# Optimization experiments

Hardware: AMD Instinct MI355X
Metric: run time of the kernel (lower is better)

## Reference

```python
import jax, jax.numpy as jnp
import numpy as np

TAU = 1.0
SCALE = 0.5
LN_EPS = 1e-5
NORM_EPS = 1e-12


def setup_inputs() -> dict:
    key = jax.random.key(0)
    k1, = jax.random.split(key, 1)
    N, D = 16384, 128
    x = jax.random.normal(k1, (N, D), dtype=jnp.float32)
    gamma = jnp.ones((D,), dtype=jnp.float32)
    beta = jnp.zeros((D,), dtype=jnp.float32)
    return {"x": x, "gamma": gamma, "beta": beta}


def reference(x, gamma, beta):
    # 'cn' branch: row-normalize, full pairwise cosine sim, row softmax, aggregate
    norm = jnp.sqrt(jnp.sum(x * x, axis=1, keepdims=True))
    norm_x = x / jnp.maximum(norm, NORM_EPS)          # [N, D]
    sim = jax.nn.softmax(norm_x @ norm_x.T / TAU, axis=1)  # [N, N]
    x_neg = sim @ x                                    # [N, D]
    y = (1.0 + SCALE) * x - SCALE * x_neg
    # LayerNorm over the hidden dim
    mu = jnp.mean(y, axis=-1, keepdims=True)
    var = jnp.mean((y - mu) ** 2, axis=-1, keepdims=True)
    return (y - mu) * jax.lax.rsqrt(var + LN_EPS) * gamma + beta
```

## Files before the change

### kernel.cpp

```cpp
#include <hip/hip_runtime.h>
#include <stdint.h>

#define NN 16384
#define DD 128
#define KT 64
#define QB 128
#define VSTR 72
#define VBYTES 9216

typedef float f32x16 __attribute__((ext_vector_type(16)));
typedef int i32x8 __attribute__((ext_vector_type(8)));

using gv = __attribute__((address_space(1))) const void;
using lv = __attribute__((address_space(3))) void;

__device__ __forceinline__ i32x8 mk8(uint4 a, uint4 b) {
  i32x8 r;
  r[0] = a.x; r[1] = a.y; r[2] = a.z; r[3] = a.w;
  r[4] = b.x; r[5] = b.y; r[6] = b.z; r[7] = b.w;
  return r;
}

#define MFMA64(A, B, C) \
  __builtin_amdgcn_mfma_scale_f32_32x32x64_f8f6f4((A), (B), (C), 0, 0, 0, 0x7F7F7F7F, 0, 0x7F7F7F7F)

__global__ void k_norm(const float* __restrict__ x, uint8_t* __restrict__ nx) {
  const int wave = threadIdx.x >> 6, lane = threadIdx.x & 63;
  const int row = blockIdx.x * 4 + wave;
  const float2 v = *reinterpret_cast<const float2*>(x + (size_t)row * DD + 2 * lane);
  float ss = v.x * v.x + v.y * v.y;
#pragma unroll
  for (int m = 1; m < 64; m <<= 1) ss += __shfl_xor(ss, m);
  const float rn = 1.2011224087f / fmaxf(sqrtf(ss), 1e-12f);
  const int w = __builtin_amdgcn_cvt_pk_fp8_f32(v.x * rn, v.y * rn, 0, false);
  *reinterpret_cast<uint16_t*>(nx + (size_t)row * DD + 2 * lane) = (uint16_t)w;
}

__global__ void k_transpose(const float* __restrict__ x, uint8_t* __restrict__ xT) {
  __shared__ uint16_t tile[64 * 66];
  const int n0 = blockIdx.x * 64;
  const int t = threadIdx.x;
#pragma unroll
  for (int e = 0; e < 16; ++e) {
    const int idx = e * 256 + t;
    const int r = idx >> 6, c2 = idx & 63;
    const float2 v = *reinterpret_cast<const float2*>(x + (size_t)(n0 + r) * DD + 2 * c2);
    const int w = __builtin_amdgcn_cvt_pk_fp8_f32(v.x, v.y, 0, false);
    tile[r * 66 + c2] = (uint16_t)w;
  }
  __syncthreads();
  const uint8_t* t8 = reinterpret_cast<const uint8_t*>(tile);
#pragma unroll
  for (int e = 0; e < 8; ++e) {
    const int idx = e * 256 + t;
    const int d = idx >> 4, n4 = (idx & 15) << 2;
    uint32_t w = (uint32_t)t8[(n4 + 0) * 132 + d];
    w |= (uint32_t)t8[(n4 + 1) * 132 + d] << 8;
    w |= (uint32_t)t8[(n4 + 2) * 132 + d] << 16;
    w |= (uint32_t)t8[(n4 + 3) * 132 + d] << 24;
    *reinterpret_cast<uint32_t*>(xT + (size_t)d * NN + n0 + n4) = w;
  }
}

template <int NSPLIT>
__global__ __launch_bounds__(256, 3) void k_attn(
    const uint8_t* __restrict__ nx, const uint8_t* __restrict__ xT,
    float* __restrict__ Op, float* __restrict__ Lp) {
  __shared__ alignas(16) uint8_t Vb[2][VBYTES];

  const int tid = threadIdx.x;
  const int wave = tid >> 6;
  const int lane = tid & 63;
  const int rl = lane & 31;
  const int hi = lane >> 5;

  const int id = blockIdx.x;
  const int split = id >> 7;
  const int qblock = id & 127;

  constexpr int qtn = 256 / NSPLIT;
  constexpr int rem = 256 % NSPLIT;
  const int nt = qtn + (split < rem ? 1 : 0);
  const int t0s = split * qtn + (split < rem ? split : rem);

  const int qw = qblock * QB + wave * 32;

  const int j0 = 2 * wave;
  const int cnt = (wave == 3) ? 3 : 2;
  uint32_t soff[3];
#pragma unroll
  for (int i = 0; i < 3; ++i) {
    const int j = j0 + i;
    const int t16 = j * 64 + lane;
    const int d = (2 * t16) / 9;
    const int c0 = t16 * 16 - d * VSTR;
    soff[i] = (uint32_t)(d * NN + c0 + (c0 >= 64 ? (NN - VSTR) : 0));
  }

  auto stage = [&](int tt, int buf) {
    const uint8_t* basep = xT + tt * KT;
#pragma unroll
    for (int i = 0; i < 3; ++i)
      if (i < cnt)
        __builtin_amdgcn_global_load_lds((gv*)(basep + soff[i]),
            (lv*)(&Vb[buf][0] + (j0 + i) * 1024), 16, 0, 0);
  };

  const uint8_t* qrow = nx + (size_t)(qw + rl) * DD + 32 * hi;
  i32x8 q8[2];
#pragma unroll
  for (int c = 0; c < 2; ++c)
    q8[c] = mk8(*reinterpret_cast<const uint4*>(qrow + c * 64),
                *reinterpret_cast<const uint4*>(qrow + c * 64 + 16));

  f32x16 o[4];
#pragma unroll
  for (int dt = 0; dt < 4; ++dt)
#pragma unroll
    for (int r = 0; r < 16; ++r) o[dt][r] = 0.f;
  float lsum = 0.f;

  stage(t0s, 0);

  for (int t = 0; t < nt; ++t) {
    const int buf = t & 1;
    __builtin_amdgcn_sched_barrier(0);
    asm volatile("s_waitcnt vmcnt(0)" ::: "memory");
    __builtin_amdgcn_sched_barrier(0);
    __builtin_amdgcn_s_barrier();
    __builtin_amdgcn_sched_barrier(0);
    if (t + 1 < nt) stage(t0s + t + 1, buf ^ 1);

    const int k0 = (t0s + t) * KT;
    const uint8_t* vb = &Vb[buf][0];
    const uint8_t* kgp = nx + (size_t)k0 * DD + (size_t)rl * DD + 32 * hi;

    uint32_t W0[4], W1[4];
#pragma unroll
    for (int kt = 0; kt < 2; ++kt) {
      const uint8_t* kp = kgp + kt * 32 * DD;
      const i32x8 ka0 = mk8(*reinterpret_cast<const uint4*>(kp),
                            *reinterpret_cast<const uint4*>(kp + 16));
      const i32x8 ka1 = mk8(*reinterpret_cast<const uint4*>(kp + 64),
                            *reinterpret_cast<const uint4*>(kp + 80));
      f32x16 s = {};
      __builtin_amdgcn_s_setprio(1);
      s = MFMA64(ka0, q8[0], s);
      s = MFMA64(ka1, q8[1], s);
      __builtin_amdgcn_s_setprio(0);
      float e[16];
#pragma unroll
      for (int r = 0; r < 16; ++r) {
        float p;
        asm("v_exp_f32 %0, %1" : "=v"(p) : "v"(s[r]));
        e[r] = p;
        lsum += p;
      }
      uint32_t* W = kt ? W1 : W0;
#pragma unroll
      for (int g = 0; g < 4; ++g) {
        uint32_t w = (uint32_t)__builtin_amdgcn_cvt_pk_fp8_f32(e[4 * g + 0], e[4 * g + 1], 0, false);
        w = (uint32_t)__builtin_amdgcn_cvt_pk_fp8_f32(e[4 * g + 2], e[4 * g + 3], (int)w, true);
        W[g] = w;
      }
    }
#pragma unroll
    for (int g = 0; g < 4; ++g)
      asm("v_permlane32_swap_b32 %0, %1" : "+v"(W0[g]), "+v"(W1[g]));
    i32x8 pa;
    pa[0] = (int)W0[0]; pa[1] = (int)W1[0]; pa[2] = (int)W0[1]; pa[3] = (int)W1[1];
    pa[4] = (int)W0[2]; pa[5] = (int)W1[2]; pa[6] = (int)W0[3]; pa[7] = (int)W1[3];

    __builtin_amdgcn_s_setprio(1);
#pragma unroll
    for (int dt = 0; dt < 4; ++dt) {
      const uint8_t* vp = vb + (dt * 32 + rl) * VSTR + 32 * hi;
      const i32x8 vf = mk8(*reinterpret_cast<const uint4*>(vp),
                           *reinterpret_cast<const uint4*>(vp + 16));
      o[dt] = MFMA64(pa, vf, o[dt]);
    }
    __builtin_amdgcn_s_setprio(0);
  }

  const float lt = lsum + __shfl_xor(lsum, 32);
  if (hi == 0) Lp[(size_t)split * NN + qw + rl] = lt;

  float* Ob = Op + (size_t)split * NN * DD;
#pragma unroll
  for (int dt = 0; dt < 4; ++dt)
#pragma unroll
    for (int r = 0; r < 16; ++r) {
      const int q = (r & 3) + 8 * (r >> 2) + 4 * hi;
      Ob[(size_t)(qw + q) * DD + dt * 32 + rl] = o[dt][r];
    }
}

__global__ void k_final(const float* __restrict__ x, const float* __restrict__ gamma,
                        const float* __restrict__ beta, const float* __restrict__ Op,
                        const float* __restrict__ Lp, float* __restrict__ out, int nsplit) {
  const int wave = threadIdx.x >> 6, lane = threadIdx.x & 63;
  const int row = blockIdx.x * 4 + wave;
  float o0 = 0.f, o1 = 0.f, lt = 0.f;
  for (int s = 0; s < nsplit; ++s) {
    const float2 v = *reinterpret_cast<const float2*>(
        Op + (size_t)s * NN * DD + (size_t)row * DD + 2 * lane);
    o0 += v.x;
    o1 += v.y;
    lt += Lp[(size_t)s * NN + row];
  }
  const float inv = 1.0f / lt;
  const float2 xv = *reinterpret_cast<const float2*>(x + (size_t)row * DD + 2 * lane);
  float y0 = 1.5f * xv.x - 0.5f * o0 * inv;
  float y1 = 1.5f * xv.y - 0.5f * o1 * inv;
  float sum = y0 + y1;
#pragma unroll
  for (int m = 1; m < 64; m <<= 1) sum += __shfl_xor(sum, m);
  const float mu = sum * (1.0f / 128.0f);
  const float d0 = y0 - mu, d1 = y1 - mu;
  float vs = d0 * d0 + d1 * d1;
#pragma unroll
  for (int m = 1; m < 64; m <<= 1) vs += __shfl_xor(vs, m);
  const float rs = rsqrtf(vs * (1.0f / 128.0f) + 1e-5f);
  const float2 g = *reinterpret_cast<const float2*>(gamma + 2 * lane);
  const float2 b = *reinterpret_cast<const float2*>(beta + 2 * lane);
  float2 ov;
  ov.x = d0 * rs * g.x + b.x;
  ov.y = d1 * rs * g.y + b.y;
  *reinterpret_cast<float2*>(out + (size_t)row * DD + 2 * lane) = ov;
}

extern "C" void kernel_launch(void* const* d_in, const int* in_sizes, int n_in,
                              void* d_out, int out_size, void* d_ws, size_t ws_size,
                              hipStream_t stream) {
  const float* x = (const float*)d_in[0];
  const float* gamma = (const float*)d_in[1];
  const float* beta = (const float*)d_in[2];
  float* out = (float*)d_out;
  char* ws = (char*)d_ws;

  uint8_t* nx = (uint8_t*)ws;
  uint8_t* xT = (uint8_t*)(ws + (size_t)NN * DD);
  const size_t base = (size_t)2 * NN * DD;
  const size_t per = (size_t)NN * DD * 4 + (size_t)NN * 4;

  int nsplit = 2;
  if (ws_size >= base + 6 * per) nsplit = 6;
  else if (ws_size >= base + 4 * per) nsplit = 4;

  float* Op = (float*)(ws + base);
  float* Lp = (float*)(ws + base + (size_t)nsplit * NN * DD * 4);

  k_norm<<<NN / 4, 256, 0, stream>>>(x, nx);
  k_transpose<<<NN / 64, 256, 0, stream>>>(x, xT);
  if (nsplit == 6)
    k_attn<6><<<dim3(128 * 6), 256, 0, stream>>>(nx, xT, Op, Lp);
  else if (nsplit == 4)
    k_attn<4><<<dim3(128 * 4), 256, 0, stream>>>(nx, xT, Op, Lp);
  else
    k_attn<2><<<dim3(128 * 2), 256, 0, stream>>>(nx, xT, Op, Lp);
  k_final<<<NN / 4, 256, 0, stream>>>(x, gamma, beta, Op, Lp, out, nsplit);
}
```

Measured before the change: 163.0 us.

## Stage K tiles through LDS, raise occupancy, use 8 splits with grouped block mapping

Each K tile is now brought into a double-buffered LDS buffer with global_load_lds alongside the V tile. Two waves stage K while the other two stage V, so the per-wave global fragment loads in the inner loop go away. Occupancy in launch bounds goes from 3 to 4, the split-K count goes from 6 to 8 with a block index mapping that groups splits of the same query block together, and the setprio hints are removed. This doubles LDS use per block and could hurt if the extra LDS traffic or the larger partial-output reduction outweighs the gain in reuse.

New measurement: 165.6 us. Within noise of the previous version (+1.6%).

```diff
diff --git a/kernel.cpp b/kernel.cpp
--- a/kernel.cpp
+++ b/kernel.cpp
@@ -5,7 +5,9 @@
 #define DD 128
 #define KT 64
 #define QB 128
+#define KSTR 144
 #define VSTR 72
+#define KBYTES 9216
 #define VBYTES 9216
 
 typedef float f32x16 __attribute__((ext_vector_type(16)));
@@ -63,9 +65,10 @@
 }
 
 template <int NSPLIT>
-__global__ __launch_bounds__(256, 3) void k_attn(
+__global__ __launch_bounds__(256, 4) void k_attn(
     const uint8_t* __restrict__ nx, const uint8_t* __restrict__ xT,
     float* __restrict__ Op, float* __restrict__ Lp) {
+  __shared__ alignas(16) uint8_t Kb[2][KBYTES];
   __shared__ alignas(16) uint8_t Vb[2][VBYTES];
 
   const int tid = threadIdx.x;
@@ -75,35 +78,40 @@
   const int hi = lane >> 5;
 
   const int id = blockIdx.x;
-  const int split = id >> 7;
-  const int qblock = id & 127;
-
-  constexpr int qtn = 256 / NSPLIT;
-  constexpr int rem = 256 % NSPLIT;
-  const int nt = qtn + (split < rem ? 1 : 0);
-  const int t0s = split * qtn + (split < rem ? split : rem);
-
+  constexpr int gs = 8 / NSPLIT;
+  const int split = (id & 7) / gs;
+  const int qblock = (id >> 3) * gs + (id & (gs - 1));
+
+  constexpr int nt = 256 / NSPLIT;
+  const int t0s = split * nt;
   const int qw = qblock * QB + wave * 32;
 
-  const int j0 = 2 * wave;
-  const int cnt = (wave == 3) ? 3 : 2;
-  uint32_t soff[3];
-#pragma unroll
-  for (int i = 0; i < 3; ++i) {
+  const int sw = wave >> 1;
+  const int j0 = (wave & 1) * 5;
+  const int cnt = (wave & 1) ? 4 : 5;
+  uint32_t soff[5];
+#pragma unroll
+  for (int i = 0; i < 5; ++i) {
     const int j = j0 + i;
     const int t16 = j * 64 + lane;
-    const int d = (2 * t16) / 9;
-    const int c0 = t16 * 16 - d * VSTR;
-    soff[i] = (uint32_t)(d * NN + c0 + (c0 >= 64 ? (NN - VSTR) : 0));
+    if (sw == 0) {
+      soff[i] = (uint32_t)((t16 / 9) * DD + (t16 % 9) * 16);
+    } else {
+      const int d = (2 * t16) / 9;
+      const int c0 = t16 * 16 - d * VSTR;
+      soff[i] = (uint32_t)(d * NN + c0 + (c0 >= 64 ? (NN - VSTR) : 0));
+    }
   }
 
   auto stage = [&](int tt, int buf) {
-    const uint8_t* basep = xT + tt * KT;
-#pragma unroll
-    for (int i = 0; i < 3; ++i)
+    const int k0 = tt * KT;
+    const uint8_t* basep = (sw == 0) ? (nx + (size_t)k0 * DD) : (xT + k0);
+    uint8_t* ldsb = (sw == 0) ? &Kb[buf][0] : &Vb[buf][0];
+#pragma unroll
+    for (int i = 0; i < 5; ++i)
       if (i < cnt)
         __builtin_amdgcn_global_load_lds((gv*)(basep + soff[i]),
-            (lv*)(&Vb[buf][0] + (j0 + i) * 1024), 16, 0, 0);
+            (lv*)(ldsb + (j0 + i) * 1024), 16, 0, 0);
   };
 
   const uint8_t* qrow = nx + (size_t)(qw + rl) * DD + 32 * hi;
@@ -131,23 +139,20 @@
     __builtin_amdgcn_sched_barrier(0);
     if (t + 1 < nt) stage(t0s + t + 1, buf ^ 1);
 
-    const int k0 = (t0s + t) * KT;
+    const uint8_t* kb = &Kb[buf][0];
     const uint8_t* vb = &Vb[buf][0];
-    const uint8_t* kgp = nx + (size_t)k0 * DD + (size_t)rl * DD + 32 * hi;
 
     uint32_t W0[4], W1[4];
 #pragma unroll
     for (int kt = 0; kt < 2; ++kt) {
-      const uint8_t* kp = kgp + kt * 32 * DD;
-      const i32x8 ka0 = mk8(*reinterpret_cast<const uint4*>(kp),
-                            *reinterpret_cast<const uint4*>(kp + 16));
-      const i32x8 ka1 = mk8(*reinterpret_cast<const uint4*>(kp + 64),
-                            *reinterpret_cast<const uint4*>(kp + 80));
+      const uint8_t* kbb = kb + kt * 32 * KSTR + rl * KSTR + 32 * hi;
+      const i32x8 ka0 = mk8(*reinterpret_cast<const uint4*>(kbb),
+                            *reinterpret_cast<const uint4*>(kbb + 16));
+      const i32x8 ka1 = mk8(*reinterpret_cast<const uint4*>(kbb + 64),
+                            *reinterpret_cast<const uint4*>(kbb + 80));
       f32x16 s = {};
-      __builtin_amdgcn_s_setprio(1);
       s = MFMA64(ka0, q8[0], s);
       s = MFMA64(ka1, q8[1], s);
-      __builtin_amdgcn_s_setprio(0);
       float e[16];
 #pragma unroll
       for (int r = 0; r < 16; ++r) {
@@ -171,7 +176,6 @@
     pa[0] = (int)W0[0]; pa[1] = (int)W1[0]; pa[2] = (int)W0[1]; pa[3] = (int)W1[1];
     pa[4] = (int)W0[2]; pa[5] = (int)W1[2]; pa[6] = (int)W0[3]; pa[7] = (int)W1[3];
 
-    __builtin_amdgcn_s_setprio(1);
 #pragma unroll
     for (int dt = 0; dt < 4; ++dt) {
       const uint8_t* vp = vb + (dt * 32 + rl) * VSTR + 32 * hi;
@@ -179,7 +183,6 @@
                            *reinterpret_cast<const uint4*>(vp + 16));
       o[dt] = MFMA64(pa, vf, o[dt]);
     }
-    __builtin_amdgcn_s_setprio(0);
   }
 
   const float lt = lsum + __shfl_xor(lsum, 32);
@@ -244,7 +247,7 @@
   const size_t per = (size_t)NN * DD * 4 + (size_t)NN * 4;
 
   int nsplit = 2;
-  if (ws_size >= base + 6 * per) nsplit = 6;
+  if (ws_size >= base + 8 * per) nsplit = 8;
   else if (ws_size >= base + 4 * per) nsplit = 4;
 
   float* Op = (float*)(ws + base);
@@ -252,8 +255,8 @@
 
   k_norm<<<NN / 4, 256, 0, stream>>>(x, nx);
   k_transpose<<<NN / 64, 256, 0, stream>>>(x, xT);
-  if (nsplit == 6)
-    k_attn<6><<<dim3(128 * 6), 256, 0, stream>>>(nx, xT, Op, Lp);
+  if (nsplit == 8)
+    k_attn<8><<<dim3(128 * 8), 256, 0, stream>>>(nx, xT, Op, Lp);
   else if (nsplit == 4)
     k_attn<4><<<dim3(128 * 4), 256, 0, stream>>>(nx, xT, Op, Lp);
   else
```
